# Kernel tuning notes

Hardware: AMD Instinct MI355X
Metric: run time of the kernel (lower is better)

Reference implementation:

```python
import jax, jax.numpy as jnp
import numpy as np

B, C, H, W = 8, 32, 256, 448


def setup_inputs() -> dict:
    key = jax.random.key(0)
    k1, k2 = jax.random.split(key)
    input1 = jax.random.normal(k1, (B, C, H, W), dtype=jnp.float32)
    input2 = jax.random.normal(k2, (B, 2, H, W), dtype=jnp.float32)  # flow (u, v)
    return {"input1": input1, "input2": input2, "kernel_size": 1}


def _forward_splat(input1, input2):
    """Forward warp: splat each source pixel to (x+u, y+v) with bilinear weights,
    accumulating via scatter-add (kernel_size=1 -> 2x2 bilinear footprint)."""
    b, c, h, w = input1.shape
    u = input2[:, 0]  # [B,H,W] horizontal flow
    v = input2[:, 1]  # [B,H,W] vertical flow
    xs = jnp.arange(w, dtype=input2.dtype)
    ys = jnp.arange(h, dtype=input2.dtype)
    tx = xs[None, None, :] + u  # target x, [B,H,W]
    ty = ys[None, :, None] + v  # target y, [B,H,W]
    x0 = jnp.floor(tx).astype(jnp.int32)
    y0 = jnp.floor(ty).astype(jnp.int32)
    fx = tx - x0.astype(tx.dtype)
    fy = ty - y0.astype(ty.dtype)

    vals = input1.transpose(0, 2, 3, 1).reshape(b * h * w, c)  # [BHW, C]
    out = jnp.zeros((b * h * w, c), dtype=input1.dtype)
    batch_off = (jnp.arange(b, dtype=jnp.int32) * (h * w))[:, None, None]

    for dx, dy in ((0, 0), (1, 0), (0, 1), (1, 1)):
        xx = x0 + dx
        yy = y0 + dy
        wx = fx if dx == 1 else (1.0 - fx)
        wy = fy if dy == 1 else (1.0 - fy)
        wgt = wx * wy  # [B,H,W]
        valid = (xx >= 0) & (xx < w) & (yy >= 0) & (yy < h)
        wgt = jnp.where(valid, wgt, 0.0)
        idx = batch_off + jnp.clip(yy, 0, h - 1) * w + jnp.clip(xx, 0, w - 1)
        out = out.at[idx.reshape(-1)].add(wgt.reshape(-1, 1) * vals)

    return out.reshape(b, h, w, c).transpose(0, 3, 1, 2)


def reference(input1, input2, kernel_size):
    # kernel_size=1 corresponds to the standard bilinear (2x2) splat footprint.
    return _forward_splat(input1, input2)
```

## Files before the change

### kernel.cpp

```cpp
#include <hip/hip_runtime.h>
#include <hip/hip_fp16.h>

constexpr int B = 8;
constexpr int C = 32;
constexpr int H = 256;
constexpr int W = 448;
constexpr int HW = H * W;

constexpr int TW  = 32;
constexpr int TH  = 8;
constexpr int RAD = 3;
constexpr int WX  = TW + 2 * RAD;
constexpr int WY  = TH + 2 * RAD;
constexpr int NSRC = WX * WY;
constexpr int NT  = 256;
constexpr int SITER = (NSRC + NT - 1) / NT;

static __device__ __forceinline__ unsigned pkrtz(float a, float b) {
    return __builtin_bit_cast(unsigned, __builtin_amdgcn_cvt_pkrtz(a, b));
}

static __device__ __forceinline__ __half2 h2(unsigned u) {
    union { unsigned u; __half2 h; } x;
    x.u = u;
    return x.h;
}

__global__ __launch_bounds__(NT)
void splat_out(const float* __restrict__ in1,
               const float* __restrict__ flow,
               float* __restrict__ out,
               unsigned* __restrict__ wcnt,
               unsigned* __restrict__ wlist,
               unsigned cap) {
    __shared__ unsigned long long mAllS[NT];
    __shared__ unsigned long long mDxS[NT];
    __shared__ unsigned long long mDyS[NT];
    __shared__ uint2 geomW[NSRC];
    __shared__ uint4 valV[2 * NSRC];

    int bid = blockIdx.x;
    int b = bid & 7;
    int t = bid >> 3;
    int ty = t / 14;
    int tx = t - ty * 14;
    int ox = tx * TW, oy = ty * TH;
    int tid = threadIdx.x;
    int qlx = tid & 31, qly = tid >> 5;
    int qx = ox + qlx, qy = oy + qly;

    mAllS[tid] = 0ull;
    mDxS[tid] = 0ull;
    mDyS[tid] = 0ull;
    __syncthreads();

    int sg[SITER];
    const int fbase = b * 2 * HW;
#pragma unroll
    for (int j = 0; j < SITER; ++j) {
        int i = tid + j * NT;
        if (i < NSRC) {
            int wy = i / WX, wx = i - wy * WX;
            int sx = ox + wx - RAD, sy = oy + wy - RAD;
            int cx = min(max(sx, 0), W - 1), cy = min(max(sy, 0), H - 1);
            int g = cy * W + cx;
            sg[j] = g;
            uint2 wd = make_uint2(0u, 0u);
            if (sx == cx && sy == cy) {
                float u = flow[fbase + g];
                float v = flow[fbase + g + HW];
                float txf = (float)sx + u;
                float tyf = (float)sy + v;
                float x0f = floorf(txf), y0f = floorf(tyf);
                int rx = (int)x0f - sx, ry = (int)y0f - sy;
                if (rx >= -RAD && rx <= RAD - 1 && ry >= -RAD && ry <= RAD - 1) {
                    float fx = txf - x0f, fy = tyf - y0f;
                    wd.x = pkrtz((1.f - fx) * (1.f - fy), fx * (1.f - fy));
                    wd.y = pkrtz((1.f - fx) * fy,         fx * fy);
                    int lx0 = wx + rx;
                    int ly0 = wy + ry;
#pragma unroll
                    for (int corner = 0; corner < 4; ++corner) {
                        int dxx = corner & 1, dyy = corner >> 1;
                        int ccx = lx0 + dxx - RAD;
                        int ccy = ly0 + dyy - RAD;
                        if ((unsigned)ccx < (unsigned)TW &&
                            (unsigned)ccy < (unsigned)TH) {
                            int cell = ccy * TW + ccx;
                            unsigned long long bit =
                                1ull << ((3 - (ry + dyy)) * 8 + (3 - (rx + dxx)));
                            atomicOr(&mAllS[cell], bit);
                            if (dxx) atomicOr(&mDxS[cell], bit);
                            if (dyy) atomicOr(&mDyS[cell], bit);
                        }
                    }
                } else if (wx >= RAD && wx < RAD + TW && wy >= RAD && wy < RAD + TH) {
                    unsigned slot = atomicAdd(wcnt, 1u);
                    if (slot < cap) wlist[slot] = ((unsigned)b << 17) | (unsigned)g;
                }
            }
            geomW[i] = wd;
        } else {
            sg[j] = -1;
        }
    }

    const float* inb = in1 + (size_t)b * C * HW;

    auto stage = [&](int pass) {
#pragma unroll
        for (int j = 0; j < SITER; ++j) {
            int i = tid + j * NT;
            if (i < NSRC) {
                const float* p = inb + sg[j] + (size_t)(16 * pass) * HW;
                valV[2 * i] = make_uint4(
                    pkrtz(p[0],               p[(size_t)HW]),
                    pkrtz(p[(size_t)2 * HW],  p[(size_t)3 * HW]),
                    pkrtz(p[(size_t)4 * HW],  p[(size_t)5 * HW]),
                    pkrtz(p[(size_t)6 * HW],  p[(size_t)7 * HW]));
                const float* p8 = p + (size_t)8 * HW;
                valV[2 * i + 1] = make_uint4(
                    pkrtz(p8[0],              p8[(size_t)HW]),
                    pkrtz(p8[(size_t)2 * HW], p8[(size_t)3 * HW]),
                    pkrtz(p8[(size_t)4 * HW], p8[(size_t)5 * HW]),
                    pkrtz(p8[(size_t)6 * HW], p8[(size_t)7 * HW]));
            }
        }
    };

    stage(0);
    __syncthreads();

    const unsigned long long m0  = mAllS[tid];
    const unsigned long long mdx = mDxS[tid];
    const unsigned long long mdy = mDyS[tid];
    const int qbase = (qly + RAD) * WX + (qlx + RAD);
    float* outp = out + (size_t)b * C * HW + qy * W + qx;

    auto gather = [&](float* o) {
        __half2 acc2[8];
#pragma unroll
        for (int k = 0; k < 8; ++k) acc2[k] = h2(0u);
        unsigned long long m = m0;
        if (m) {
            int j = (int)__builtin_ctzll(m); m &= m - 1;
            int wi = qbase + ((j >> 3) - 3) * WX + ((j & 7) - 3);
            uint2 wdc = geomW[wi];
            uint4 va = valV[2 * wi];
            uint4 vb = valV[2 * wi + 1];
            unsigned dxx = (unsigned)(mdx >> j) & 1u;
            unsigned dyy = (unsigned)(mdy >> j) & 1u;
            while (m) {
                int jn = (int)__builtin_ctzll(m); m &= m - 1;
                int win = qbase + ((jn >> 3) - 3) * WX + ((jn & 7) - 3);
                uint2 wdn = geomW[win];
                uint4 van = valV[2 * win];
                uint4 vbn = valV[2 * win + 1];
                unsigned dxxn = (unsigned)(mdx >> jn) & 1u;
                unsigned dyyn = (unsigned)(mdy >> jn) & 1u;
                unsigned wd = dyy ? wdc.y : wdc.x;
                unsigned hq = (wd >> (16u * dxx)) & 0xFFFFu;
                __half2 w2 = h2(hq | (hq << 16));
                acc2[0] = __hfma2(h2(va.x), w2, acc2[0]);
                acc2[1] = __hfma2(h2(va.y), w2, acc2[1]);
                acc2[2] = __hfma2(h2(va.z), w2, acc2[2]);
                acc2[3] = __hfma2(h2(va.w), w2, acc2[3]);
                acc2[4] = __hfma2(h2(vb.x), w2, acc2[4]);
                acc2[5] = __hfma2(h2(vb.y), w2, acc2[5]);
                acc2[6] = __hfma2(h2(vb.z), w2, acc2[6]);
                acc2[7] = __hfma2(h2(vb.w), w2, acc2[7]);
                wdc = wdn; va = van; vb = vbn; dxx = dxxn; dyy = dyyn;
            }
            unsigned wd = dyy ? wdc.y : wdc.x;
            unsigned hq = (wd >> (16u * dxx)) & 0xFFFFu;
            __half2 w2 = h2(hq | (hq << 16));
            acc2[0] = __hfma2(h2(va.x), w2, acc2[0]);
            acc2[1] = __hfma2(h2(va.y), w2, acc2[1]);
            acc2[2] = __hfma2(h2(va.z), w2, acc2[2]);
            acc2[3] = __hfma2(h2(va.w), w2, acc2[3]);
            acc2[4] = __hfma2(h2(vb.x), w2, acc2[4]);
            acc2[5] = __hfma2(h2(vb.y), w2, acc2[5]);
            acc2[6] = __hfma2(h2(vb.z), w2, acc2[6]);
            acc2[7] = __hfma2(h2(vb.w), w2, acc2[7]);
        }
#pragma unroll
        for (int k = 0; k < 8; ++k) {
            float2 f = __half22float2(acc2[k]);
            o[(size_t)(2 * k) * HW]     = f.x;
            o[(size_t)(2 * k + 1) * HW] = f.y;
        }
    };

    gather(outp);
    __syncthreads();
    stage(1);
    __syncthreads();
    gather(outp + (size_t)16 * HW);
}

__global__ void outlier_list(const float* __restrict__ in1,
                             const float* __restrict__ flow,
                             float* __restrict__ out,
                             const unsigned* __restrict__ wcnt,
                             const unsigned* __restrict__ wlist,
                             unsigned cap) {
    unsigned n = *wcnt;
    if (n > cap) return;
    unsigned total = n * 8u;
    for (unsigned idx = blockIdx.x * blockDim.x + threadIdx.x;
         idx < total; idx += gridDim.x * blockDim.x) {
        unsigned e = wlist[idx >> 3];
        int c0 = (int)(idx & 7u) * 4;
        int bb = (int)(e >> 17);
        int p  = (int)(e & 0x1FFFFu);
        int y = p / W, x = p - y * W;

        float u = flow[(bb * 2 + 0) * HW + p];
        float v = flow[(bb * 2 + 1) * HW + p];
        float txf = (float)x + u;
        float tyf = (float)y + v;
        float fx0 = floorf(txf), fy0 = floorf(tyf);
        int x0 = (int)fx0, y0 = (int)fy0;
        float fx = txf - fx0, fy = tyf - fy0;
        float w00 = (1.0f - fx) * (1.0f - fy);
        float w10 = fx * (1.0f - fy);
        float w01 = (1.0f - fx) * fy;
        float w11 = fx * fy;
        bool vx0 = (x0 >= 0) && (x0 < W);
        bool vx1 = (x0 + 1 >= 0) && (x0 + 1 < W);
        bool vy0 = (y0 >= 0) && (y0 < H);
        bool vy1 = (y0 + 1 >= 0) && (y0 + 1 < H);
        long o00 = (long)y0 * W + x0;

        const float* src  = in1 + (size_t)bb * C * HW + (size_t)c0 * HW + p;
        float*       dstb = out + (size_t)bb * C * HW + (size_t)c0 * HW;
        for (int c = 0; c < 4; ++c) {
            float val = src[(size_t)c * HW];
            float* ob = dstb + (size_t)c * HW;
            if (vx0 && vy0) atomicAdd(ob + o00,         w00 * val);
            if (vx1 && vy0) atomicAdd(ob + o00 + 1,     w10 * val);
            if (vx0 && vy1) atomicAdd(ob + o00 + W,     w01 * val);
            if (vx1 && vy1) atomicAdd(ob + o00 + W + 1, w11 * val);
        }
    }
}

__global__ void outlier_fallback(const float* __restrict__ in1,
                                 const float* __restrict__ flow,
                                 float* __restrict__ out,
                                 const unsigned* __restrict__ wcnt,
                                 unsigned cap) {
    if (*wcnt <= cap) return;
    int npix = B * HW;
    for (int idx = blockIdx.x * blockDim.x + threadIdx.x;
         idx < npix; idx += gridDim.x * blockDim.x) {
        int b = idx / HW;
        int p = idx - b * HW;
        int y = p / W, x = p - y * W;
        float u = flow[(b * 2 + 0) * HW + p];
        float v = flow[(b * 2 + 1) * HW + p];
        float txf = (float)x + u;
        float tyf = (float)y + v;
        float fx0 = floorf(txf), fy0 = floorf(tyf);
        int x0 = (int)fx0, y0 = (int)fy0;
        int rx = x0 - x, ry = y0 - y;
        bool handled = (rx >= -RAD) && (rx <= RAD - 1) &&
                       (ry >= -RAD) && (ry <= RAD - 1);
        if (handled) continue;
        float fx = txf - fx0, fy = tyf - fy0;
        float w00 = (1.0f - fx) * (1.0f - fy);
        float w10 = fx * (1.0f - fy);
        float w01 = (1.0f - fx) * fy;
        float w11 = fx * fy;
        bool vx0 = (x0 >= 0) && (x0 < W);
        bool vx1 = (x0 + 1 >= 0) && (x0 + 1 < W);
        bool vy0 = (y0 >= 0) && (y0 < H);
        bool vy1 = (y0 + 1 >= 0) && (y0 + 1 < H);
        long o00 = (long)y0 * W + x0;
        const float* src = in1 + (size_t)b * C * HW + p;
        float* dstb = out + (size_t)b * C * HW;
        for (int c = 0; c < C; ++c) {
            float val = src[(size_t)c * HW];
            float* ob = dstb + (size_t)c * HW;
            if (vx0 && vy0) atomicAdd(ob + o00,         w00 * val);
            if (vx1 && vy0) atomicAdd(ob + o00 + 1,     w10 * val);
            if (vx0 && vy1) atomicAdd(ob + o00 + W,     w01 * val);
            if (vx1 && vy1) atomicAdd(ob + o00 + W + 1, w11 * val);
        }
    }
}

extern "C" void kernel_launch(void* const* d_in, const int* in_sizes, int n_in,
                              void* d_out, int out_size, void* d_ws, size_t ws_size,
                              hipStream_t stream) {
    const float* in1  = (const float*)d_in[0];
    const float* flow = (const float*)d_in[1];
    float* out = (float*)d_out;

    unsigned* wcnt  = (unsigned*)d_ws;
    unsigned* wlist = wcnt + 4;
    unsigned cap = 0;
    if (ws_size >= 64) {
        size_t c = ws_size / sizeof(unsigned) - 4;
        cap = (c > 0x7FFFFFFFull) ? 0x7FFFFFFFu : (unsigned)c;
    }

    hipMemsetAsync(wcnt, 0, sizeof(unsigned), stream);

    int nblocks = B * (H / TH) * (W / TW);
    splat_out<<<nblocks, NT, 0, stream>>>(in1, flow, out, wcnt, wlist, cap);

    outlier_list<<<256, 256, 0, stream>>>(in1, flow, out, wcnt, wlist, cap);
    outlier_fallback<<<256, 256, 0, stream>>>(in1, flow, out, wcnt, cap);
}
```

Measured before the change: 112.9 us.

## Stage source values with float4 loads into channel-planar LDS; merge outlier kernels

Widens the source window to 40 columns aligned to 4 so input channels are staged with coalesced float4 loads, packed to fp16 pairs, and stored channel-plane-major in shared memory. Gather now reads 8 separate unsigned LDS words per contributor instead of two uint4s, and the software-pipelined prefetch is dropped. The two outlier kernels become one, saving a launch. The changes aim at the cost of scalar strided global loads during staging, in exchange for more LDS reads in the gather and extra halo columns.

```diff
diff --git a/kernel.cpp b/kernel.cpp
--- a/kernel.cpp
+++ b/kernel.cpp
@@ -10,11 +10,14 @@
 constexpr int TW  = 32;
 constexpr int TH  = 8;
 constexpr int RAD = 3;
-constexpr int WX  = TW + 2 * RAD;
+constexpr int WXV = 40;
 constexpr int WY  = TH + 2 * RAD;
-constexpr int NSRC = WX * WY;
+constexpr int NV  = WXV * WY;
 constexpr int NT  = 256;
-constexpr int SITER = (NSRC + NT - 1) / NT;
+constexpr int GITER = (NV + NT - 1) / NT;
+constexpr int NG4 = (WXV / 4) * WY;
+constexpr int NITEM = NG4 * 8;
+constexpr int KITER = (NITEM + NT - 1) / NT;
 
 static __device__ __forceinline__ unsigned pkrtz(float a, float b) {
     return __builtin_bit_cast(unsigned, __builtin_amdgcn_cvt_pkrtz(a, b));
@@ -36,8 +39,8 @@
     __shared__ unsigned long long mAllS[NT];
     __shared__ unsigned long long mDxS[NT];
     __shared__ unsigned long long mDyS[NT];
-    __shared__ uint2 geomW[NSRC];
-    __shared__ uint4 valV[2 * NSRC];
+    __shared__ uint2    geomW[NV];
+    __shared__ unsigned valV[8 * NV];
 
     int bid = blockIdx.x;
     int b = bid & 7;
@@ -50,40 +53,36 @@
     int qx = ox + qlx, qy = oy + qly;
 
     mAllS[tid] = 0ull;
-    mDxS[tid] = 0ull;
-    mDyS[tid] = 0ull;
-    __syncthreads();
-
-    int sg[SITER];
+    mDxS[tid]  = 0ull;
+    mDyS[tid]  = 0ull;
+    __syncthreads();
+
     const int fbase = b * 2 * HW;
 #pragma unroll
-    for (int j = 0; j < SITER; ++j) {
-        int i = tid + j * NT;
-        if (i < NSRC) {
-            int wy = i / WX, wx = i - wy * WX;
-            int sx = ox + wx - RAD, sy = oy + wy - RAD;
-            int cx = min(max(sx, 0), W - 1), cy = min(max(sy, 0), H - 1);
-            int g = cy * W + cx;
-            sg[j] = g;
+    for (int k = 0; k < GITER; ++k) {
+        int i = tid + k * NT;
+        if (i < NV) {
+            int wy = i / WXV, wv = i - wy * WXV;
+            int gx = ox + wv - 4;
+            int sy = oy + wy - RAD;
             uint2 wd = make_uint2(0u, 0u);
-            if (sx == cx && sy == cy) {
+            if ((unsigned)gx < (unsigned)W && (unsigned)sy < (unsigned)H) {
+                int g = sy * W + gx;
                 float u = flow[fbase + g];
                 float v = flow[fbase + g + HW];
-                float txf = (float)sx + u;
+                float txf = (float)gx + u;
                 float tyf = (float)sy + v;
                 float x0f = floorf(txf), y0f = floorf(tyf);
-                int rx = (int)x0f - sx, ry = (int)y0f - sy;
+                int rx = (int)x0f - gx, ry = (int)y0f - sy;
                 if (rx >= -RAD && rx <= RAD - 1 && ry >= -RAD && ry <= RAD - 1) {
                     float fx = txf - x0f, fy = tyf - y0f;
                     wd.x = pkrtz((1.f - fx) * (1.f - fy), fx * (1.f - fy));
                     wd.y = pkrtz((1.f - fx) * fy,         fx * fy);
-                    int lx0 = wx + rx;
-                    int ly0 = wy + ry;
 #pragma unroll
                     for (int corner = 0; corner < 4; ++corner) {
                         int dxx = corner & 1, dyy = corner >> 1;
-                        int ccx = lx0 + dxx - RAD;
-                        int ccy = ly0 + dyy - RAD;
+                        int ccx = gx + rx + dxx - ox;
+                        int ccy = sy + ry + dyy - oy;
                         if ((unsigned)ccx < (unsigned)TW &&
                             (unsigned)ccy < (unsigned)TH) {
                             int cell = ccy * TW + ccx;
@@ -94,14 +93,13 @@
                             if (dyy) atomicOr(&mDyS[cell], bit);
                         }
                     }
-                } else if (wx >= RAD && wx < RAD + TW && wy >= RAD && wy < RAD + TH) {
+                } else if (wv >= 4 && wv < 4 + TW &&
+                           wy >= RAD && wy < RAD + TH) {
                     unsigned slot = atomicAdd(wcnt, 1u);
                     if (slot < cap) wlist[slot] = ((unsigned)b << 17) | (unsigned)g;
                 }
             }
             geomW[i] = wd;
-        } else {
-            sg[j] = -1;
         }
     }
 
@@ -109,21 +107,25 @@
 
     auto stage = [&](int pass) {
 #pragma unroll
-        for (int j = 0; j < SITER; ++j) {
-            int i = tid + j * NT;
-            if (i < NSRC) {
-                const float* p = inb + sg[j] + (size_t)(16 * pass) * HW;
-                valV[2 * i] = make_uint4(
-                    pkrtz(p[0],               p[(size_t)HW]),
-                    pkrtz(p[(size_t)2 * HW],  p[(size_t)3 * HW]),
-                    pkrtz(p[(size_t)4 * HW],  p[(size_t)5 * HW]),
-                    pkrtz(p[(size_t)6 * HW],  p[(size_t)7 * HW]));
-                const float* p8 = p + (size_t)8 * HW;
-                valV[2 * i + 1] = make_uint4(
-                    pkrtz(p8[0],              p8[(size_t)HW]),
-                    pkrtz(p8[(size_t)2 * HW], p8[(size_t)3 * HW]),
-                    pkrtz(p8[(size_t)4 * HW], p8[(size_t)5 * HW]),
-                    pkrtz(p8[(size_t)6 * HW], p8[(size_t)7 * HW]));
+        for (int k = 0; k < KITER; ++k) {
+            int id = tid + k * NT;
+            if (id < NITEM) {
+                int g4 = id % NG4;
+                int cp = id / NG4;
+                int wy = g4 / (WXV / 4);
+                int wv4 = (g4 - wy * (WXV / 4)) * 4;
+                int row = min(max(oy + wy - RAD, 0), H - 1);
+                int gxb = min(max(ox + wv4 - 4, 0), W - 4);
+                const float* base = inb + (size_t)(16 * pass + 2 * cp) * HW
+                                        + (size_t)row * W + gxb;
+                float4 a = *reinterpret_cast<const float4*>(base);
+                float4 c = *reinterpret_cast<const float4*>(base + (size_t)HW);
+                uint4 wv_;
+                wv_.x = pkrtz(a.x, c.x);
+                wv_.y = pkrtz(a.y, c.y);
+                wv_.z = pkrtz(a.z, c.z);
+                wv_.w = pkrtz(a.w, c.w);
+                *reinterpret_cast<uint4*>(&valV[cp * NV + wy * WXV + wv4]) = wv_;
             }
         }
     };
@@ -134,7 +136,7 @@
     const unsigned long long m0  = mAllS[tid];
     const unsigned long long mdx = mDxS[tid];
     const unsigned long long mdy = mDyS[tid];
-    const int qbase = (qly + RAD) * WX + (qlx + RAD);
+    const int qbase = (qly + RAD) * WXV + (qlx + 4);
     float* outp = out + (size_t)b * C * HW + qy * W + qx;
 
     auto gather = [&](float* o) {
@@ -142,46 +144,24 @@
 #pragma unroll
         for (int k = 0; k < 8; ++k) acc2[k] = h2(0u);
         unsigned long long m = m0;
-        if (m) {
-            int j = (int)__builtin_ctzll(m); m &= m - 1;
-            int wi = qbase + ((j >> 3) - 3) * WX + ((j & 7) - 3);
-            uint2 wdc = geomW[wi];
-            uint4 va = valV[2 * wi];
-            uint4 vb = valV[2 * wi + 1];
+        while (m) {
+            int j = (int)__builtin_ctzll(m);
+            m &= m - 1;
+            int wi = qbase + ((j >> 3) - 3) * WXV + ((j & 7) - 3);
             unsigned dxx = (unsigned)(mdx >> j) & 1u;
             unsigned dyy = (unsigned)(mdy >> j) & 1u;
-            while (m) {
-                int jn = (int)__builtin_ctzll(m); m &= m - 1;
-                int win = qbase + ((jn >> 3) - 3) * WX + ((jn & 7) - 3);
-                uint2 wdn = geomW[win];
-                uint4 van = valV[2 * win];
-                uint4 vbn = valV[2 * win + 1];
-                unsigned dxxn = (unsigned)(mdx >> jn) & 1u;
-                unsigned dyyn = (unsigned)(mdy >> jn) & 1u;
-                unsigned wd = dyy ? wdc.y : wdc.x;
-                unsigned hq = (wd >> (16u * dxx)) & 0xFFFFu;
-                __half2 w2 = h2(hq | (hq << 16));
-                acc2[0] = __hfma2(h2(va.x), w2, acc2[0]);
-                acc2[1] = __hfma2(h2(va.y), w2, acc2[1]);
-                acc2[2] = __hfma2(h2(va.z), w2, acc2[2]);
-                acc2[3] = __hfma2(h2(va.w), w2, acc2[3]);
-                acc2[4] = __hfma2(h2(vb.x), w2, acc2[4]);
-                acc2[5] = __hfma2(h2(vb.y), w2, acc2[5]);
-                acc2[6] = __hfma2(h2(vb.z), w2, acc2[6]);
-                acc2[7] = __hfma2(h2(vb.w), w2, acc2[7]);
-                wdc = wdn; va = van; vb = vbn; dxx = dxxn; dyy = dyyn;
-            }
-            unsigned wd = dyy ? wdc.y : wdc.x;
+            uint2 wd2 = geomW[wi];
+            unsigned wd = dyy ? wd2.y : wd2.x;
             unsigned hq = (wd >> (16u * dxx)) & 0xFFFFu;
             __half2 w2 = h2(hq | (hq << 16));
-            acc2[0] = __hfma2(h2(va.x), w2, acc2[0]);
-            acc2[1] = __hfma2(h2(va.y), w2, acc2[1]);
-            acc2[2] = __hfma2(h2(va.z), w2, acc2[2]);
-            acc2[3] = __hfma2(h2(va.w), w2, acc2[3]);
-            acc2[4] = __hfma2(h2(vb.x), w2, acc2[4]);
-            acc2[5] = __hfma2(h2(vb.y), w2, acc2[5]);
-            acc2[6] = __hfma2(h2(vb.z), w2, acc2[6]);
-            acc2[7] = __hfma2(h2(vb.w), w2, acc2[7]);
+            acc2[0] = __hfma2(h2(valV[0 * NV + wi]), w2, acc2[0]);
+            acc2[1] = __hfma2(h2(valV[1 * NV + wi]), w2, acc2[1]);
+            acc2[2] = __hfma2(h2(valV[2 * NV + wi]), w2, acc2[2]);
+            acc2[3] = __hfma2(h2(valV[3 * NV + wi]), w2, acc2[3]);
+            acc2[4] = __hfma2(h2(valV[4 * NV + wi]), w2, acc2[4]);
+            acc2[5] = __hfma2(h2(valV[5 * NV + wi]), w2, acc2[5]);
+            acc2[6] = __hfma2(h2(valV[6 * NV + wi]), w2, acc2[6]);
+            acc2[7] = __hfma2(h2(valV[7 * NV + wi]), w2, acc2[7]);
         }
 #pragma unroll
         for (int k = 0; k < 8; ++k) {
@@ -198,94 +178,88 @@
     gather(outp + (size_t)16 * HW);
 }
 
-__global__ void outlier_list(const float* __restrict__ in1,
-                             const float* __restrict__ flow,
-                             float* __restrict__ out,
-                             const unsigned* __restrict__ wcnt,
-                             const unsigned* __restrict__ wlist,
-                             unsigned cap) {
-    unsigned n = *wcnt;
-    if (n > cap) return;
-    unsigned total = n * 8u;
-    for (unsigned idx = blockIdx.x * blockDim.x + threadIdx.x;
-         idx < total; idx += gridDim.x * blockDim.x) {
-        unsigned e = wlist[idx >> 3];
-        int c0 = (int)(idx & 7u) * 4;
-        int bb = (int)(e >> 17);
-        int p  = (int)(e & 0x1FFFFu);
-        int y = p / W, x = p - y * W;
-
-        float u = flow[(bb * 2 + 0) * HW + p];
-        float v = flow[(bb * 2 + 1) * HW + p];
-        float txf = (float)x + u;
-        float tyf = (float)y + v;
-        float fx0 = floorf(txf), fy0 = floorf(tyf);
-        int x0 = (int)fx0, y0 = (int)fy0;
-        float fx = txf - fx0, fy = tyf - fy0;
-        float w00 = (1.0f - fx) * (1.0f - fy);
-        float w10 = fx * (1.0f - fy);
-        float w01 = (1.0f - fx) * fy;
-        float w11 = fx * fy;
-        bool vx0 = (x0 >= 0) && (x0 < W);
-        bool vx1 = (x0 + 1 >= 0) && (x0 + 1 < W);
-        bool vy0 = (y0 >= 0) && (y0 < H);
-        bool vy1 = (y0 + 1 >= 0) && (y0 + 1 < H);
-        long o00 = (long)y0 * W + x0;
-
-        const float* src  = in1 + (size_t)bb * C * HW + (size_t)c0 * HW + p;
-        float*       dstb = out + (size_t)bb * C * HW + (size_t)c0 * HW;
-        for (int c = 0; c < 4; ++c) {
-            float val = src[(size_t)c * HW];
-            float* ob = dstb + (size_t)c * HW;
-            if (vx0 && vy0) atomicAdd(ob + o00,         w00 * val);
-            if (vx1 && vy0) atomicAdd(ob + o00 + 1,     w10 * val);
-            if (vx0 && vy1) atomicAdd(ob + o00 + W,     w01 * val);
-            if (vx1 && vy1) atomicAdd(ob + o00 + W + 1, w11 * val);
-        }
-    }
-}
-
-__global__ void outlier_fallback(const float* __restrict__ in1,
+__global__ void outlier_combined(const float* __restrict__ in1,
                                  const float* __restrict__ flow,
                                  float* __restrict__ out,
                                  const unsigned* __restrict__ wcnt,
+                                 const unsigned* __restrict__ wlist,
                                  unsigned cap) {
-    if (*wcnt <= cap) return;
-    int npix = B * HW;
-    for (int idx = blockIdx.x * blockDim.x + threadIdx.x;
-         idx < npix; idx += gridDim.x * blockDim.x) {
-        int b = idx / HW;
-        int p = idx - b * HW;
-        int y = p / W, x = p - y * W;
-        float u = flow[(b * 2 + 0) * HW + p];
-        float v = flow[(b * 2 + 1) * HW + p];
-        float txf = (float)x + u;
-        float tyf = (float)y + v;
-        float fx0 = floorf(txf), fy0 = floorf(tyf);
-        int x0 = (int)fx0, y0 = (int)fy0;
-        int rx = x0 - x, ry = y0 - y;
-        bool handled = (rx >= -RAD) && (rx <= RAD - 1) &&
-                       (ry >= -RAD) && (ry <= RAD - 1);
-        if (handled) continue;
-        float fx = txf - fx0, fy = tyf - fy0;
-        float w00 = (1.0f - fx) * (1.0f - fy);
-        float w10 = fx * (1.0f - fy);
-        float w01 = (1.0f - fx) * fy;
-        float w11 = fx * fy;
-        bool vx0 = (x0 >= 0) && (x0 < W);
-        bool vx1 = (x0 + 1 >= 0) && (x0 + 1 < W);
-        bool vy0 = (y0 >= 0) && (y0 < H);
-        bool vy1 = (y0 + 1 >= 0) && (y0 + 1 < H);
-        long o00 = (long)y0 * W + x0;
-        const float* src = in1 + (size_t)b * C * HW + p;
-        float* dstb = out + (size_t)b * C * HW;
-        for (int c = 0; c < C; ++c) {
-            float val = src[(size_t)c * HW];
-            float* ob = dstb + (size_t)c * HW;
-            if (vx0 && vy0) atomicAdd(ob + o00,         w00 * val);
-            if (vx1 && vy0) atomicAdd(ob + o00 + 1,     w10 * val);
-            if (vx0 && vy1) atomicAdd(ob + o00 + W,     w01 * val);
-            if (vx1 && vy1) atomicAdd(ob + o00 + W + 1, w11 * val);
+    unsigned n = *wcnt;
+    if (n <= cap) {
+        unsigned total = n * 8u;
+        for (unsigned idx = blockIdx.x * blockDim.x + threadIdx.x;
+             idx < total; idx += gridDim.x * blockDim.x) {
+            unsigned e = wlist[idx >> 3];
+            int c0 = (int)(idx & 7u) * 4;
+            int bb = (int)(e >> 17);
+            int p  = (int)(e & 0x1FFFFu);
+            int y = p / W, x = p - y * W;
+
+            float u = flow[(bb * 2 + 0) * HW + p];
+            float v = flow[(bb * 2 + 1) * HW + p];
+            float txf = (float)x + u;
+            float tyf = (float)y + v;
+            float fx0 = floorf(txf), fy0 = floorf(tyf);
+            int x0 = (int)fx0, y0 = (int)fy0;
+            float fx = txf - fx0, fy = tyf - fy0;
+            float w00 = (1.0f - fx) * (1.0f - fy);
+            float w10 = fx * (1.0f - fy);
+            float w01 = (1.0f - fx) * fy;
+            float w11 = fx * fy;
+            bool vx0 = (x0 >= 0) && (x0 < W);
+            bool vx1 = (x0 + 1 >= 0) && (x0 + 1 < W);
+            bool vy0 = (y0 >= 0) && (y0 < H);
+            bool vy1 = (y0 + 1 >= 0) && (y0 + 1 < H);
+            long o00 = (long)y0 * W + x0;
+
+            const float* src  = in1 + (size_t)bb * C * HW + (size_t)c0 * HW + p;
+            float*       dstb = out + (size_t)bb * C * HW + (size_t)c0 * HW;
+            for (int c = 0; c < 4; ++c) {
+                float val = src[(size_t)c * HW];
+                float* ob = dstb + (size_t)c * HW;
+                if (vx0 && vy0) atomicAdd(ob + o00,         w00 * val);
+                if (vx1 && vy0) atomicAdd(ob + o00 + 1,     w10 * val);
+                if (vx0 && vy1) atomicAdd(ob + o00 + W,     w01 * val);
+                if (vx1 && vy1) atomicAdd(ob + o00 + W + 1, w11 * val);
+            }
+        }
+    } else {
+        int npix = B * HW;
+        for (int idx = blockIdx.x * blockDim.x + threadIdx.x;
+             idx < npix; idx += gridDim.x * blockDim.x) {
+            int b = idx / HW;
+            int p = idx - b * HW;
+            int y = p / W, x = p - y * W;
+            float u = flow[(b * 2 + 0) * HW + p];
+            float v = flow[(b * 2 + 1) * HW + p];
+            float txf = (float)x + u;
+            float tyf = (float)y + v;
+            float fx0 = floorf(txf), fy0 = floorf(tyf);
+            int x0 = (int)fx0, y0 = (int)fy0;
+            int rx = x0 - x, ry = y0 - y;
+            bool handled = (rx >= -RAD) && (rx <= RAD - 1) &&
+                           (ry >= -RAD) && (ry <= RAD - 1);
+            if (handled) continue;
+            float fx = txf - fx0, fy = tyf - fy0;
+            float w00 = (1.0f - fx) * (1.0f - fy);
+            float w10 = fx * (1.0f - fy);
+            float w01 = (1.0f - fx) * fy;
+            float w11 = fx * fy;
+            bool vx0 = (x0 >= 0) && (x0 < W);
+            bool vx1 = (x0 + 1 >= 0) && (x0 + 1 < W);
+            bool vy0 = (y0 >= 0) && (y0 < H);
+            bool vy1 = (y0 + 1 >= 0) && (y0 + 1 < H);
+            long o00 = (long)y0 * W + x0;
+            const float* src = in1 + (size_t)b * C * HW + p;
+            float* dstb = out + (size_t)b * C * HW;
+            for (int c = 0; c < C; ++c) {
+                float val = src[(size_t)c * HW];
+                float* ob = dstb + (size_t)c * HW;
+                if (vx0 && vy0) atomicAdd(ob + o00,         w00 * val);
+                if (vx1 && vy0) atomicAdd(ob + o00 + 1,     w10 * val);
+                if (vx0 && vy1) atomicAdd(ob + o00 + W,     w01 * val);
+                if (vx1 && vy1) atomicAdd(ob + o00 + W + 1, w11 * val);
+            }
         }
     }
 }
@@ -310,6 +284,5 @@
     int nblocks = B * (H / TH) * (W / TW);
     splat_out<<<nblocks, NT, 0, stream>>>(in1, flow, out, wcnt, wlist, cap);
 
-    outlier_list<<<256, 256, 0, stream>>>(in1, flow, out, wcnt, wlist, cap);
-    outlier_fallback<<<256, 256, 0, stream>>>(in1, flow, out, wcnt, cap);
-}
+    outlier_combined<<<256, 256, 0, stream>>>(in1, flow, out, wcnt, wlist, cap);
+}
```

New measurement: 111.6 us. Within noise of the previous version (-1.1%).
